# Kernel tuning notes

Measured on AMD Instinct MI355X. Metric: run time of the kernel, lower is better.

The kernel has to match this reference:

```python
import jax, jax.numpy as jnp
import numpy as np

B, N, M, K = 4, 20000, 20000, 16
C_IN, C_MID, C_ADD = 64, 16, 3


def setup_inputs() -> dict:
    key = jax.random.key(0)
    k1, k2, k3, k4 = jax.random.split(key, 4)
    input_features = jax.random.normal(k1, (B, N, C_IN), dtype=jnp.float32)
    neighbor_inds = jax.random.randint(k2, (B, M, K), 0, N, dtype=jnp.int64)
    weightnet = jax.random.normal(k3, (B, M, K, C_MID), dtype=jnp.float32)
    additional_features = jax.random.normal(k4, (B, M, K, C_ADD), dtype=jnp.float32)
    return {
        "input_features": input_features,
        "neighbor_inds": neighbor_inds,
        "weightnet": weightnet,
        "additional_features": additional_features,
    }


def reference(input_features, neighbor_inds, weightnet, additional_features):
    # Gather neighbor features: [B, M, K, C_in]
    gathered = jax.vmap(lambda feats, inds: feats[inds])(input_features, neighbor_inds)
    # Concat extra per-neighbor features: [B, M, K, C_in + C_add]
    feats = jnp.concatenate([gathered, additional_features], axis=-1)
    # Per-point contraction over K neighbors: [B, M, C_in+C_add, C_mid]
    out = jnp.einsum("bmkc,bmkw->bmcw", feats, weightnet)
    b, m = out.shape[0], out.shape[1]
    return out.reshape(b, m, -1)  # [B, M, (C_in+C_add)*C_mid]
```

## Files before the change

kernel.cpp:

```cpp
#include <hip/hip_runtime.h>

#define B_    4
#define N_    20000
#define M_    20000
#define K_    16
#define CIN   64
#define CMID  16
#define COUT  67
#define PPB   4
#define LSTR  17
#define NXCD  8

typedef float float4_ __attribute__((ext_vector_type(4)));

__global__ __launch_bounds__(256, 6) void pconv_kernel(
    const float* __restrict__ in_feats,
    const int*   __restrict__ inds,
    const float* __restrict__ wn,
    const float* __restrict__ addl,
    float*       __restrict__ out)
{
    __shared__ float lds_out[PPB][(COUT + 1) * LSTR];
    __shared__ float lds_wn [PPB][K_ * CMID];

    const int tid  = threadIdx.x;
    const int lane = tid & 63;
    const int wav  = tid >> 6;

    const int nwg  = gridDim.x;
    const int q_   = nwg / NXCD;
    const int swz  = (blockIdx.x % NXCD) * q_ + blockIdx.x / NXCD;

    int bp = __builtin_amdgcn_readfirstlane(swz * PPB + wav);
    const int b = bp / M_;

    const int*   pinds = inds + bp * K_;
    const float* pwn   = wn   + (long)bp * (K_ * CMID);
    const float* padd  = addl + (long)bp * (K_ * 3);
    const float* bfeat = in_feats + (long)b * N_ * CIN;

    float4_ wstage = ((const float4_*)pwn)[lane];

    int idxs[K_];
    #pragma unroll
    for (int k = 0; k < K_; ++k) idxs[k] = pinds[k];

    float f[K_];
    #pragma unroll
    for (int k = 0; k < K_; ++k)
        f[k] = bfeat[(long)idxs[k] * CIN + lane];

    *(float4_*)(&lds_wn[wav][lane * 4]) = wstage;

    float acc[CMID];
    #pragma unroll
    for (int w = 0; w < CMID; ++w) acc[w] = 0.f;

    #pragma unroll
    for (int k = 0; k < K_; ++k) {
        const float* lw = &lds_wn[wav][k * CMID];
        float4_ w0 = *(const float4_*)(lw + 0);
        float4_ w1 = *(const float4_*)(lw + 4);
        float4_ w2 = *(const float4_*)(lw + 8);
        float4_ w3 = *(const float4_*)(lw + 12);
        #pragma unroll
        for (int e = 0; e < 4; ++e) {
            acc[0  + e] += f[k] * w0[e];
            acc[4  + e] += f[k] * w1[e];
            acc[8  + e] += f[k] * w2[e];
            acc[12 + e] += f[k] * w3[e];
        }
    }

    float* lo = &lds_out[wav][0];
    #pragma unroll
    for (int w = 0; w < CMID; ++w)
        lo[lane * LSTR + w] = acc[w];

    const int t  = lane >> 4;
    const int wt = lane & 15;
    if (lane < 48) {
        float acc2 = 0.f;
        #pragma unroll
        for (int k = 0; k < K_; ++k) {
            float a0 = padd[k * 3 + 0];
            float a1 = padd[k * 3 + 1];
            float a2 = padd[k * 3 + 2];
            float av = (t == 0) ? a0 : (t == 1) ? a1 : a2;
            acc2 += av * lds_wn[wav][k * CMID + wt];
        }
        lo[(CIN + t) * LSTR + wt] = acc2;
    }

    float* pout = out + (long)bp * (COUT * CMID);
    const int q = lane >> 2;
    const int r = lane & 3;
    #pragma unroll
    for (int p = 0; p < 4; ++p) {
        const float* src = lo + (p * 16 + q) * LSTR + 4 * r;
        float4_ v = { src[0], src[1], src[2], src[3] };
        *(float4_*)(pout + p * 256 + lane * 4) = v;
    }
    if (lane < 12) {
        const float* src = lo + (CIN + q) * LSTR + 4 * r;
        float4_ v = { src[0], src[1], src[2], src[3] };
        *(float4_*)(pout + 1024 + lane * 4) = v;
    }
}

extern "C" void kernel_launch(void* const* d_in, const int* in_sizes, int n_in,
                              void* d_out, int out_size, void* d_ws, size_t ws_size,
                              hipStream_t stream) {
    const float* in_feats = (const float*)d_in[0];
    const int*   ninds    = (const int*)d_in[1];
    const float* wn       = (const float*)d_in[2];
    const float* addl     = (const float*)d_in[3];
    float*       out      = (float*)d_out;

    const int total_points = B_ * M_;
    dim3 grid(total_points / PPB);
    dim3 block(256);
    pconv_kernel<<<grid, block, 0, stream>>>(in_feats, ninds, wn, addl, out);
}
```

Before: 129.1 us.

## Convert to persistent grid with software-pipelined prefetch of next point

Replaces one-wave-per-point launch with a fixed persistent grid. Each XCD owns a contiguous range of points, and waves stride through it. The gather, weightnet and additional-feature loads for the next point are issued before computing the current one, which is meant to hide gather latency and cut per-block launch overhead. The additional features are staged in LDS so the extra-channel contraction no longer does repeated global loads. In exchange it uses more registers for the double buffers, which can reduce occupancy.

```diff
diff --git a/kernel.cpp b/kernel.cpp
--- a/kernel.cpp
+++ b/kernel.cpp
@@ -10,6 +10,9 @@
 #define PPB   4
 #define LSTR  17
 #define NXCD  8
+#define GRID_BLOCKS 1792
+#define WPX   896
+#define PTSX  10000
 
 typedef float float4_ __attribute__((ext_vector_type(4)));
 
@@ -20,91 +23,124 @@
     const float* __restrict__ addl,
     float*       __restrict__ out)
 {
-    __shared__ float lds_out[PPB][(COUT + 1) * LSTR];
-    __shared__ float lds_wn [PPB][K_ * CMID];
+    __shared__ float lds_out [PPB][1140];
+    __shared__ float lds_wn  [PPB][K_ * CMID];
+    __shared__ float lds_addl[PPB][52];
 
     const int tid  = threadIdx.x;
     const int lane = tid & 63;
-    const int wav  = tid >> 6;
+    const int wav  = __builtin_amdgcn_readfirstlane(tid >> 6);
 
-    const int nwg  = gridDim.x;
-    const int q_   = nwg / NXCD;
-    const int swz  = (blockIdx.x % NXCD) * q_ + blockIdx.x / NXCD;
+    const int xcd = __builtin_amdgcn_readfirstlane(blockIdx.x & (NXCD - 1));
+    const int ww  = __builtin_amdgcn_readfirstlane((blockIdx.x >> 3) * PPB + wav);
+    const int pbase = xcd * PTSX;
 
-    int bp = __builtin_amdgcn_readfirstlane(swz * PPB + wav);
-    const int b = bp / M_;
+    const float* bfeat = in_feats + (long)(xcd >> 1) * N_ * CIN;
 
-    const int*   pinds = inds + bp * K_;
-    const float* pwn   = wn   + (long)bp * (K_ * CMID);
-    const float* padd  = addl + (long)bp * (K_ * 3);
-    const float* bfeat = in_feats + (long)b * N_ * CIN;
+    float   fC[K_], fN[K_];
+    float4_ wC, wN;
+    float   aC = 0.f, aN = 0.f;
+    int     idxN[K_];
 
-    float4_ wstage = ((const float4_*)pwn)[lane];
+    int p = ww;
+    if (p >= PTSX) return;
 
-    int idxs[K_];
-    #pragma unroll
-    for (int k = 0; k < K_; ++k) idxs[k] = pinds[k];
-
-    float f[K_];
-    #pragma unroll
-    for (int k = 0; k < K_; ++k)
-        f[k] = bfeat[(long)idxs[k] * CIN + lane];
-
-    *(float4_*)(&lds_wn[wav][lane * 4]) = wstage;
-
-    float acc[CMID];
-    #pragma unroll
-    for (int w = 0; w < CMID; ++w) acc[w] = 0.f;
-
-    #pragma unroll
-    for (int k = 0; k < K_; ++k) {
-        const float* lw = &lds_wn[wav][k * CMID];
-        float4_ w0 = *(const float4_*)(lw + 0);
-        float4_ w1 = *(const float4_*)(lw + 4);
-        float4_ w2 = *(const float4_*)(lw + 8);
-        float4_ w3 = *(const float4_*)(lw + 12);
+    {
+        const int bp = pbase + p;
+        const int* pi = inds + bp * K_;
+        int idx0[K_];
         #pragma unroll
-        for (int e = 0; e < 4; ++e) {
-            acc[0  + e] += f[k] * w0[e];
-            acc[4  + e] += f[k] * w1[e];
-            acc[8  + e] += f[k] * w2[e];
-            acc[12 + e] += f[k] * w3[e];
+        for (int k = 0; k < K_; ++k) idx0[k] = pi[k];
+        #pragma unroll
+        for (int k = 0; k < K_; ++k)
+            fC[k] = bfeat[(long)idx0[k] * CIN + lane];
+        wC = ((const float4_*)(wn + (long)bp * (K_ * CMID)))[lane];
+        if (lane < 48) aC = addl[(long)bp * 48 + lane];
+        if (p + WPX < PTSX) {
+            const int* pi2 = inds + (bp + WPX) * K_;
+            #pragma unroll
+            for (int k = 0; k < K_; ++k) idxN[k] = pi2[k];
         }
     }
 
-    float* lo = &lds_out[wav][0];
-    #pragma unroll
-    for (int w = 0; w < CMID; ++w)
-        lo[lane * LSTR + w] = acc[w];
+    while (true) {
+        const int  bp   = pbase + p;
+        const int  pn   = p + WPX;
+        const bool hasN = pn < PTSX;
 
-    const int t  = lane >> 4;
-    const int wt = lane & 15;
-    if (lane < 48) {
-        float acc2 = 0.f;
+        if (hasN) {
+            const int bpn = pbase + pn;
+            #pragma unroll
+            for (int k = 0; k < K_; ++k)
+                fN[k] = bfeat[(long)idxN[k] * CIN + lane];
+            wN = ((const float4_*)(wn + (long)bpn * (K_ * CMID)))[lane];
+            if (lane < 48) aN = addl[(long)bpn * 48 + lane];
+            if (pn + WPX < PTSX) {
+                const int* pi2 = inds + (bpn + WPX) * K_;
+                #pragma unroll
+                for (int k = 0; k < K_; ++k) idxN[k] = pi2[k];
+            }
+        }
+
+        *(float4_*)(&lds_wn[wav][lane * 4]) = wC;
+        if (lane < 48) lds_addl[wav][lane] = aC;
+
+        float acc[CMID];
+        #pragma unroll
+        for (int w = 0; w < CMID; ++w) acc[w] = 0.f;
+
         #pragma unroll
         for (int k = 0; k < K_; ++k) {
-            float a0 = padd[k * 3 + 0];
-            float a1 = padd[k * 3 + 1];
-            float a2 = padd[k * 3 + 2];
-            float av = (t == 0) ? a0 : (t == 1) ? a1 : a2;
-            acc2 += av * lds_wn[wav][k * CMID + wt];
+            const float* lw = &lds_wn[wav][k * CMID];
+            float4_ w0 = *(const float4_*)(lw + 0);
+            float4_ w1 = *(const float4_*)(lw + 4);
+            float4_ w2 = *(const float4_*)(lw + 8);
+            float4_ w3 = *(const float4_*)(lw + 12);
+            #pragma unroll
+            for (int e = 0; e < 4; ++e) {
+                acc[0  + e] += fC[k] * w0[e];
+                acc[4  + e] += fC[k] * w1[e];
+                acc[8  + e] += fC[k] * w2[e];
+                acc[12 + e] += fC[k] * w3[e];
+            }
         }
-        lo[(CIN + t) * LSTR + wt] = acc2;
-    }
 
-    float* pout = out + (long)bp * (COUT * CMID);
-    const int q = lane >> 2;
-    const int r = lane & 3;
-    #pragma unroll
-    for (int p = 0; p < 4; ++p) {
-        const float* src = lo + (p * 16 + q) * LSTR + 4 * r;
-        float4_ v = { src[0], src[1], src[2], src[3] };
-        *(float4_*)(pout + p * 256 + lane * 4) = v;
-    }
-    if (lane < 12) {
-        const float* src = lo + (CIN + q) * LSTR + 4 * r;
-        float4_ v = { src[0], src[1], src[2], src[3] };
-        *(float4_*)(pout + 1024 + lane * 4) = v;
+        float* lo = &lds_out[wav][0];
+        #pragma unroll
+        for (int w = 0; w < CMID; ++w)
+            lo[lane * LSTR + w] = acc[w];
+
+        const int t  = lane >> 4;
+        const int wt = lane & 15;
+        if (lane < 48) {
+            float acc2 = 0.f;
+            #pragma unroll
+            for (int k = 0; k < K_; ++k)
+                acc2 += lds_addl[wav][k * 3 + t] * lds_wn[wav][k * CMID + wt];
+            lo[(CIN + t) * LSTR + wt] = acc2;
+        }
+
+        float* pout = out + (long)bp * (COUT * CMID);
+        const int q = lane >> 2;
+        const int r = lane & 3;
+        #pragma unroll
+        for (int pp = 0; pp < 4; ++pp) {
+            const float* src = lo + (pp * 16 + q) * LSTR + 4 * r;
+            float4_ v = { src[0], src[1], src[2], src[3] };
+            *(float4_*)(pout + pp * 256 + lane * 4) = v;
+        }
+        if (lane < 12) {
+            const float* src = lo + (CIN + q) * LSTR + 4 * r;
+            float4_ v = { src[0], src[1], src[2], src[3] };
+            *(float4_*)(pout + 1024 + lane * 4) = v;
+        }
+
+        if (!hasN) break;
+        p = pn;
+        #pragma unroll
+        for (int k = 0; k < K_; ++k) fC[k] = fN[k];
+        wC = wN;
+        aC = aN;
     }
 }
 
@@ -117,8 +153,7 @@
     const float* addl     = (const float*)d_in[3];
     float*       out      = (float*)d_out;
 
-    const int total_points = B_ * M_;
-    dim3 grid(total_points / PPB);
+    dim3 grid(GRID_BLOCKS);
     dim3 block(256);
     pconv_kernel<<<grid, block, 0, stream>>>(in_feats, ninds, wn, addl, out);
 }
```

Measured after the change: 288.8 us. +123.7%, slower.
